# Performance work log

Measured on AMD Instinct MI355X. Metric: run time of the kernel, lower is better.

## Reference

```python
import jax, jax.numpy as jnp
import numpy as np

DIM = 256
NUM_HEADS = 4
HEAD_DIM = DIM // NUM_HEADS
LN_EPS = 1e-5


def setup_inputs() -> dict:
    key = jax.random.key(0)
    ks = jax.random.split(key, 5)
    B, C, H, W = 4, DIM, 64, 64
    x = jax.random.normal(ks[0], (B, C, H, W), dtype=jnp.float32)
    ln_g = jnp.ones((DIM,), dtype=jnp.float32)
    ln_b = jnp.zeros((DIM,), dtype=jnp.float32)
    # torch Linear init scale ~ 1/sqrt(fan_in)
    w_qkv = jax.random.normal(ks[1], (DIM, 3 * DIM), dtype=jnp.float32) / np.sqrt(DIM)
    w_proj = jax.random.normal(ks[2], (DIM, DIM), dtype=jnp.float32) / np.sqrt(DIM)
    b_proj = jax.random.normal(ks[3], (DIM,), dtype=jnp.float32) * 0.01
    return {"x": x, "ln_g": ln_g, "ln_b": ln_b, "w_qkv": w_qkv,
            "w_proj": w_proj, "b_proj": b_proj}


def _attention_block(x, ln_g, ln_b, w_qkv, w_proj, b_proj):
    B, C, H, W = x.shape
    N = H * W
    h, d = NUM_HEADS, HEAD_DIM
    # b c h w -> b n c
    t = x.reshape(B, C, N).transpose(0, 2, 1)
    # LayerNorm over channel dim
    mu = jnp.mean(t, axis=-1, keepdims=True)
    var = jnp.mean(jnp.square(t - mu), axis=-1, keepdims=True)
    t = (t - mu) * jax.lax.rsqrt(var + LN_EPS) * ln_g + ln_b
    # qkv projection (no bias); layout of last dim is (three, heads, d)
    qkv = t @ w_qkv  # [B, N, 3*C]
    qkv = qkv.reshape(B, N, 3, h, d)
    q = qkv[:, :, 0].transpose(0, 2, 1, 3)  # [B, h, N, d]
    k = qkv[:, :, 1].transpose(0, 2, 1, 3)
    v = qkv[:, :, 2].transpose(0, 2, 1, 3)
    # scaled dot-product attention (original chunks over queries; same math)
    scale = 1.0 / jnp.sqrt(jnp.asarray(d, dtype=q.dtype))
    dots = jnp.einsum('bhnd,bhmd->bhnm', q, k) * scale
    attn = jax.nn.softmax(dots, axis=-1)
    o = jnp.einsum('bhnm,bhmd->bhnd', attn, v)  # [B, h, N, d]
    # b h n d -> b n (h d)
    o = o.transpose(0, 2, 1, 3).reshape(B, N, C)
    o = o @ w_proj.T + b_proj  # torch Linear convention not needed; keep explicit
    # b n c -> b c h w
    return o.transpose(0, 2, 1).reshape(B, C, H, W)


def reference(x, ln_g, ln_b, w_qkv, w_proj, b_proj):
    return _attention_block(x, ln_g, ln_b, w_qkv, w_proj, b_proj)
```

## Files before the change

kernel.cpp:

```cpp
#include <hip/hip_runtime.h>
#include <math.h>

#define NB 4
#define NC 256
#define NHEADS 4
#define DH 64
#define NT 4096
#define QSCALE (0.125f * 1.44269504088896f)

typedef __bf16  bf16x8 __attribute__((ext_vector_type(8)));
typedef float   f32x4  __attribute__((ext_vector_type(4)));
typedef float   f32x16 __attribute__((ext_vector_type(16)));
typedef short   s16x8  __attribute__((ext_vector_type(8)));
typedef unsigned int u32x4 __attribute__((ext_vector_type(4)));

static __device__ __forceinline__ unsigned short f2bf(float f) {
    unsigned u = __float_as_uint(f);
    u = (u + 0x7fffu + ((u >> 16) & 1u)) >> 16;
    return (unsigned short)u;
}

static __device__ __forceinline__ float fast_exp2(float x) {
    return __builtin_amdgcn_exp2f(x);
}

static __device__ __forceinline__ unsigned cvtpk(float lo, float hi) {
    unsigned r;
    asm("v_cvt_pk_bf16_f32 %0, %1, %2" : "=v"(r) : "v"(lo), "v"(hi));
    return r;
}

static __device__ __forceinline__ void plswap(unsigned &a, unsigned &b) {
    asm("v_permlane32_swap_b32 %0, %1" : "+v"(a), "+v"(b));
}

static __device__ __forceinline__ bf16x8 as_bf16x8(u32x4 v) {
    return __builtin_bit_cast(bf16x8, v);
}

static __device__ __forceinline__ void gload16(const unsigned short* g, unsigned short* l) {
    __builtin_amdgcn_global_load_lds((const __attribute__((address_space(1))) void*)g,
                                     (__attribute__((address_space(3))) void*)l, 16, 0, 0);
}

static __device__ __forceinline__ void stage_64x256(
    unsigned short* __restrict__ lds, const unsigned short* __restrict__ g, int tid)
{
    #pragma unroll
    for (int chunk = 0; chunk < 8; ++chunk) {
        const int row = chunk * 8 + (tid >> 5);
        const int col = (tid & 31) * 8;
        *(s16x8*)&lds[row * 264 + col] = *(const s16x8*)&g[row * 256 + col];
    }
}

__global__ __launch_bounds__(256) void k_prep(
    const float* __restrict__ wqkv, const float* __restrict__ wproj,
    unsigned short* __restrict__ wqkv_t, unsigned short* __restrict__ wproj_bf)
{
    const int id = blockIdx.x;
    const int tid = threadIdx.x;
    if (id < 48) {
        __shared__ float T[64][65];
        const int jt = id % 12, ct = id / 12;
        #pragma unroll
        for (int p = 0; p < 16; ++p) {
            const int idx = tid + (p << 8);
            const int r = idx >> 6, cl = idx & 63;
            T[r][cl] = wqkv[(size_t)(ct * 64 + r) * 768 + jt * 64 + cl];
        }
        __syncthreads();
        #pragma unroll
        for (int p = 0; p < 16; ++p) {
            const int idx = tid + (p << 8);
            const int r = idx >> 6, cl = idx & 63;
            wqkv_t[(size_t)(jt * 64 + r) * 256 + ct * 64 + cl] = f2bf(T[cl][r]);
        }
    } else {
        const int base = (id - 48) * 2048 + tid * 8;
        s16x8 v;
        #pragma unroll
        for (int j = 0; j < 8; ++j) v[j] = (short)f2bf(wproj[base + j]);
        *(s16x8*)&wproj_bf[base] = v;
    }
}

__global__ __launch_bounds__(256) void k_ln_qkv(
    const float* __restrict__ x,
    const float* __restrict__ ln_g,
    const float* __restrict__ ln_b,
    const unsigned short* __restrict__ wqkv_t,
    unsigned short* __restrict__ q_bf,
    unsigned short* __restrict__ k_bf,
    unsigned short* __restrict__ v_bf)
{
    __shared__ unsigned short An[64 * 264];
    __shared__ unsigned short Wt[64 * 264];
    __shared__ float red1[4][64], red2[4][64];
    __shared__ float mu_s[64], rs_s[64];

    const int b     = blockIdx.x >> 6;
    const int n0    = (blockIdx.x & 63) << 6;
    const int tid   = threadIdx.x;
    const int li    = tid & 63;
    const int grp   = tid >> 6;
    const int w     = grp;
    const int lane  = li;
    const int q4    = lane >> 4;
    const int c     = lane & 15;

    const float* xb = x + ((size_t)b * NC) * NT + n0 + li;

    float xr[64];
    #pragma unroll
    for (int chunk = 0; chunk < 8; ++chunk)
        #pragma unroll
        for (int j = 0; j < 8; ++j)
            xr[chunk * 8 + j] = xb[(size_t)(chunk * 32 + grp * 8 + j) * NT];

    float s1 = 0.f, s2 = 0.f;
    #pragma unroll
    for (int i = 0; i < 64; ++i) { s1 += xr[i]; s2 += xr[i] * xr[i]; }
    red1[grp][li] = s1; red2[grp][li] = s2;
    __syncthreads();
    if (tid < 64) {
        const float t1 = red1[0][tid] + red1[1][tid] + red1[2][tid] + red1[3][tid];
        const float t2 = red2[0][tid] + red2[1][tid] + red2[2][tid] + red2[3][tid];
        const float mu  = t1 * (1.0f / NC);
        const float var = t2 * (1.0f / NC) - mu * mu;
        mu_s[tid] = mu;
        rs_s[tid] = rsqrtf(var + 1e-5f);
    }
    __syncthreads();
    const float mu = mu_s[li];
    const float rs = rs_s[li];

    #pragma unroll
    for (int chunk = 0; chunk < 8; ++chunk) {
        s16x8 pk;
        #pragma unroll
        for (int j = 0; j < 8; ++j) {
            const int ch = chunk * 32 + grp * 8 + j;
            const float vv = (xr[chunk * 8 + j] - mu) * rs * ln_g[ch] + ln_b[ch];
            pk[j] = (short)f2bf(vv);
        }
        *(s16x8*)&An[li * 264 + chunk * 32 + grp * 8] = pk;
    }
    __syncthreads();

    bf16x8 aT[8];
    #pragma unroll
    for (int kt = 0; kt < 8; ++kt)
        aT[kt] = *(const bf16x8*)&An[(16 * w + c) * 264 + kt * 32 + q4 * 8];

    for (int three = 0; three < 3; ++three) {
        for (int jt = 0; jt < 4; ++jt) {
            __syncthreads();
            stage_64x256(Wt, wqkv_t + (size_t)(three * 256 + jt * 64) * 256, tid);
            __syncthreads();

            f32x4 acc[4];
            #pragma unroll
            for (int nt = 0; nt < 4; ++nt)
                #pragma unroll
                for (int r = 0; r < 4; ++r) acc[nt][r] = 0.f;

            const int bh = b * NHEADS + jt;
            if (three < 2) {
                #pragma unroll
                for (int nt = 0; nt < 4; ++nt)
                    #pragma unroll
                    for (int kt = 0; kt < 8; ++kt) {
                        const bf16x8 bb = *(const bf16x8*)&Wt[(16 * nt + c) * 264 + kt * 32 + q4 * 8];
                        acc[nt] = __builtin_amdgcn_mfma_f32_16x16x32_bf16(aT[kt], bb, acc[nt], 0, 0, 0);
                    }
                unsigned short* dst = (three == 0 ? q_bf : k_bf) + ((size_t)bh * NT + n0) * DH;
                const float sc = (three == 0) ? QSCALE : 1.0f;
                #pragma unroll
                for (int nt = 0; nt < 4; ++nt)
                    #pragma unroll
                    for (int r = 0; r < 4; ++r)
                        dst[(size_t)(16 * w + 4 * q4 + r) * DH + 16 * nt + c] = f2bf(acc[nt][r] * sc);
            } else {
                bf16x8 aW[8];
                #pragma unroll
                for (int kt = 0; kt < 8; ++kt)
                    aW[kt] = *(const bf16x8*)&Wt[(16 * w + c) * 264 + kt * 32 + q4 * 8];
                #pragma unroll
                for (int nt = 0; nt < 4; ++nt)
                    #pragma unroll
                    for (int kt = 0; kt < 8; ++kt) {
                        const bf16x8 bb = *(const bf16x8*)&An[(16 * nt + c) * 264 + kt * 32 + q4 * 8];
                        acc[nt] = __builtin_amdgcn_mfma_f32_16x16x32_bf16(aW[kt], bb, acc[nt], 0, 0, 0);
                    }
                unsigned short* dst = v_bf + (size_t)bh * DH * NT;
                #pragma unroll
                for (int nt = 0; nt < 4; ++nt)
                    #pragma unroll
                    for (int r = 0; r < 4; ++r)
                        dst[(size_t)(16 * w + 4 * q4 + r) * NT + n0 + 16 * nt + c] = f2bf(acc[nt][r]);
            }
        }
    }
}

__global__ __launch_bounds__(256, 2) void k_attn(
    const unsigned short* __restrict__ qg,
    const unsigned short* __restrict__ kg,
    const unsigned short* __restrict__ vg,
    unsigned short* __restrict__ og)
{
    __shared__ unsigned short Ks[2 * 8192];
    __shared__ unsigned short Vt[2 * 8192];
    __shared__ float l_s[4][32];

    const int bx   = ((blockIdx.x & 7) << 6) | (blockIdx.x >> 3);
    const int bh   = bx >> 5;
    const int qt   = bx & 31;
    const int n0   = qt << 7;
    const int tid  = threadIdx.x;
    const int w    = tid >> 6;
    const int lane = tid & 63;
    const int c5   = lane & 31;
    const int hi   = lane >> 5;
    const int qb   = n0 + (w << 5);
    const int swz  = c5 & 7;

    const unsigned short* kb = kg + (size_t)bh * NT * DH;
    const unsigned short* vb = vg + (size_t)bh * DH * NT;

    bf16x8 aq[4];
    {
        const unsigned short* qrow = qg + ((size_t)bh * NT + qb + c5) * DH + hi * 8;
        #pragma unroll
        for (int ks = 0; ks < 4; ++ks)
            aq[ks] = *(const bf16x8*)(qrow + ks * 16);
    }

    const int rr  = lane >> 3;
    const int kcK = (lane & 7) ^ rr;
    const int rd  = lane >> 4;
    const int ckV = lane & 15;

    #define ISSUE_TILE(it_, bi_)                                               \
        {                                                                      \
            const unsigned short* ktp = kb + (size_t)(it_) * 128 * DH;         \
            const unsigned short* vtp = vb + (size_t)(it_) * 128;              \
            _Pragma("unroll")                                                  \
            for (int t = 0; t < 4; ++t) {                                      \
                const int grp_ = w * 4 + t;                                    \
                gload16(ktp + (size_t)(grp_ * 8 + rr) * DH + kcK * 8,          \
                        &Ks[(bi_) * 8192 + grp_ * 512 + lane * 8]);            \
                const int kcV_ = ckV ^ ((4 * grp_ + rd) & 7);                  \
                gload16(vtp + (size_t)(4 * grp_ + rd) * NT + kcV_ * 8,         \
                        &Vt[(bi_) * 8192 + grp_ * 512 + lane * 8]);            \
            }                                                                  \
        }

    #define QK_SB(sv, sb)                                                      \
        {                                                                      \
            _Pragma("unroll")                                                  \
            for (int ks = 0; ks < 4; ++ks) {                                   \
                const bf16x8 kf = *(const bf16x8*)                             \
                    &Kb[((sb) * 32 + c5) * 64 + (((2 * ks + hi) ^ swz) << 3)]; \
                sv = __builtin_amdgcn_mfma_f32_32x32x16_bf16(kf, aq[ks], sv, 0, 0, 0); \
            }                                                                  \
        }

    #define EXP_SB(sv)                                                         \
        {                                                                      \
            _Pragma("unroll")                                                  \
            for (int r = 0; r < 16; r += 4) {                                  \
                sv[r]   = fast_exp2(sv[r]);   ls0 += sv[r];                    \
                sv[r+1] = fast_exp2(sv[r+1]); ls1 += sv[r+1];                  \
                sv[r+2] = fast_exp2(sv[r+2]); ls2 += sv[r+2];                  \
                sv[r+3] = fast_exp2(sv[r+3]); ls3 += sv[r+3];                  \
            }                                                                  \
        }

    #define PACK_SB(sv, pa0, pa1)                                              \
        {                                                                      \
            unsigned x0 = cvtpk(sv[0], sv[1]),  x1 = cvtpk(sv[4], sv[5]);      \
            plswap(x0, x1);                                                    \
            unsigned x2 = cvtpk(sv[2], sv[3]),  x3 = cvtpk(sv[6], sv[7]);      \
            plswap(x2, x3);                                                    \
            pa0 = (u32x4){x0, x2, x1, x3};                                     \
            unsigned y0 = cvtpk(sv[8], sv[9]),  y1 = cvtpk(sv[12], sv[13]);    \
            plswap(y0, y1);                                                    \
            unsigned y2 = cvtpk(sv[10], sv[11]), y3 = cvtpk(sv[14], sv[15]);   \
            plswap(y2, y3);                                                    \
            pa1 = (u32x4){y0, y2, y1, y3};                                     \
        }

    #define PV_SB(pa0, pa1, sb)                                                \
        {                                                                      \
            _Pragma("unroll")                                                  \
            for (int dt = 0; dt < 2; ++dt) {                                   \
                const int rv = (dt * 32 + c5) * 128;                           \
                const bf16x8 vA = *(const bf16x8*)                             \
                    &Vb[rv + (((4 * (sb) + hi) ^ swz) << 3)];                  \
                oac[dt] = __builtin_amdgcn_mfma_f32_32x32x16_bf16(             \
                    as_bf16x8(pa0), vA, oac[dt], 0, 0, 0);                     \
                const bf16x8 vB = *(const bf16x8*)                             \
                    &Vb[rv + (((4 * (sb) + 2 + hi) ^ swz) << 3)];              \
                oac[dt] = __builtin_amdgcn_mfma_f32_32x32x16_bf16(             \
                    as_bf16x8(pa1), vB, oac[dt], 0, 0, 0);                     \
            }                                                                  \
        }

    ISSUE_TILE(0, 0)

    f32x16 oac[2];
    #pragma unroll
    for (int dt = 0; dt < 2; ++dt)
        #pragma unroll
        for (int r = 0; r < 16; ++r) oac[dt][r] = 0.f;
    float ls0 = 0.f, ls1 = 0.f, ls2 = 0.f, ls3 = 0.f;

    for (int it = 0; it < 32; ++it) {
        const int cur = it & 1;
        asm volatile("s_waitcnt vmcnt(0)\n\ts_barrier" ::: "memory");
        if (it < 31) ISSUE_TILE(it + 1, cur ^ 1)

        const unsigned short* Kb = &Ks[cur * 8192];
        const unsigned short* Vb = &Vt[cur * 8192];

        f32x16 sA, sB, sC, sD;
        #pragma unroll
        for (int r = 0; r < 16; ++r) { sA[r] = 0.f; sB[r] = 0.f; sC[r] = 0.f; sD[r] = 0.f; }

        __builtin_amdgcn_s_setprio(1);
        QK_SB(sA, 0)
        QK_SB(sB, 1)
        QK_SB(sC, 2)
        QK_SB(sD, 3)
        __builtin_amdgcn_s_setprio(0);

        u32x4 a0, a1, b0, b1, c0, c1, d0, d1;
        EXP_SB(sA)
        PACK_SB(sA, a0, a1)
        EXP_SB(sB)
        PV_SB(a0, a1, 0)
        PACK_SB(sB, b0, b1)
        EXP_SB(sC)
        PV_SB(b0, b1, 1)
        PACK_SB(sC, c0, c1)
        EXP_SB(sD)
        PV_SB(c0, c1, 2)
        PACK_SB(sD, d0, d1)
        PV_SB(d0, d1, 3)
    }
    #undef ISSUE_TILE
    #undef QK_SB
    #undef EXP_SB
    #undef PACK_SB
    #undef PV_SB

    const float lsum = (ls0 + ls1) + (ls2 + ls3);
    const float t = lsum + __shfl_xor(lsum, 32);
    if (lane < 32) l_s[w][c5] = t;
    __syncthreads();

    unsigned short* ob = og + ((size_t)bh * NT + qb) * DH;
    #pragma unroll
    for (int r = 0; r < 16; ++r) {
        const int qrow = (r & 3) + 8 * (r >> 2) + 4 * hi;
        const float rn = 1.0f / l_s[w][qrow];
        ob[(size_t)qrow * DH + c5]      = f2bf(oac[0][r] * rn);
        ob[(size_t)qrow * DH + 32 + c5] = f2bf(oac[1][r] * rn);
    }
}

__global__ __launch_bounds__(256) void k_proj(
    const unsigned short* __restrict__ o_bf,
    const unsigned short* __restrict__ wproj_bf,
    const float* __restrict__ b_proj,
    float* __restrict__ out)
{
    __shared__ unsigned short Os[64 * 264];
    __shared__ unsigned short Ws[64 * 264];

    const int b   = blockIdx.x >> 6;
    const int n0  = (blockIdx.x & 63) << 6;
    const int yh  = blockIdx.y;
    const int tid = threadIdx.x;
    const int w   = tid >> 6;
    const int lane = tid & 63;
    const int q4  = lane >> 4;
    const int c   = lane & 15;

    #pragma unroll
    for (int chunk = 0; chunk < 8; ++chunk) {
        const int row = chunk * 8 + (tid >> 5);
        const int col = (tid & 31) * 8;
        const int hd  = col >> 6;
        const int c64 = col & 63;
        const unsigned short* src =
            &o_bf[((size_t)(b * NHEADS + hd) * NT + n0 + row) * DH + c64];
        *(s16x8*)&Os[row * 264 + col] = *(const s16x8*)src;
    }

    for (int ct = 0; ct < 2; ++ct) {
        const int cg0 = (yh * 2 + ct) * 64;
        if (ct) __syncthreads();
        stage_64x256(Ws, wproj_bf + (size_t)cg0 * NC, tid);
        __syncthreads();

        bf16x8 a[8];
        #pragma unroll
        for (int kt = 0; kt < 8; ++kt)
            a[kt] = *(const bf16x8*)&Ws[(16 * w + c) * 264 + kt * 32 + q4 * 8];

        f32x4 acc[4];
        #pragma unroll
        for (int nt = 0; nt < 4; ++nt)
            #pragma unroll
            for (int r = 0; r < 4; ++r) acc[nt][r] = 0.f;

        #pragma unroll
        for (int nt = 0; nt < 4; ++nt)
            #pragma unroll
            for (int kt = 0; kt < 8; ++kt) {
                const bf16x8 bb = *(const bf16x8*)&Os[(16 * nt + c) * 264 + kt * 32 + q4 * 8];
                acc[nt] = __builtin_amdgcn_mfma_f32_16x16x32_bf16(a[kt], bb, acc[nt], 0, 0, 0);
            }

        #pragma unroll
        for (int nt = 0; nt < 4; ++nt)
            #pragma unroll
            for (int r = 0; r < 4; ++r) {
                const int cg = cg0 + 16 * w + 4 * q4 + r;
                out[((size_t)b * NC + cg) * NT + n0 + 16 * nt + c] = acc[nt][r] + b_proj[cg];
            }
    }
}

extern "C" void kernel_launch(void* const* d_in, const int* in_sizes, int n_in,
                              void* d_out, int out_size, void* d_ws, size_t ws_size,
                              hipStream_t stream)
{
    const float* x      = (const float*)d_in[0];
    const float* ln_g   = (const float*)d_in[1];
    const float* ln_b   = (const float*)d_in[2];
    const float* w_qkv  = (const float*)d_in[3];
    const float* w_proj = (const float*)d_in[4];
    const float* b_proj = (const float*)d_in[5];
    float* out = (float*)d_out;

    const size_t TEN = (size_t)NB * NHEADS * NT * DH;

    unsigned short* ws16 = (unsigned short*)d_ws;
    unsigned short* q_bf    = ws16;
    unsigned short* k_bf    = ws16 + TEN;
    unsigned short* v_bf    = ws16 + 2 * TEN;
    unsigned short* o_bf    = ws16 + 3 * TEN;
    unsigned short* wqkv_t  = ws16 + 4 * TEN;
    unsigned short* wproj_b = wqkv_t + 768 * 256;

    k_prep<<<80, 256, 0, stream>>>(w_qkv, w_proj, wqkv_t, wproj_b);
    k_ln_qkv<<<NB * 64, 256, 0, stream>>>(x, ln_g, ln_b, wqkv_t, q_bf, k_bf, v_bf);
    k_attn<<<512, 256, 0, stream>>>(q_bf, k_bf, v_bf, o_bf);
    k_proj<<<dim3(NB * 64, 2), 256, 0, stream>>>(o_bf, wproj_b, b_proj, out);
}
```

Measured before the change: 182.9 us.

## Process 64 query rows per wave in attention to reuse K/V fragments

Each wave now handles two 32-row query groups, so every K and V fragment read from LDS feeds two MFMAs. The attention grid drops from 512 to 256 blocks of 256 query rows, and launch bounds change to one block per SIMD group. The goal is to halve LDS traffic and global K/V loads per unit of work. The cost is many more registers (four score accumulators, four output accumulators), lower occupancy, and only 256 blocks, which may underfill a 256-CU device with little latency hiding.

New measurement: 201.1 us. +10.0%, slower.

```diff
diff --git a/kernel.cpp b/kernel.cpp
--- a/kernel.cpp
+++ b/kernel.cpp
@@ -204,7 +204,7 @@
     }
 }
 
-__global__ __launch_bounds__(256, 2) void k_attn(
+__global__ __launch_bounds__(256, 1) void k_attn(
     const unsigned short* __restrict__ qg,
     const unsigned short* __restrict__ kg,
     const unsigned short* __restrict__ vg,
@@ -212,29 +212,31 @@
 {
     __shared__ unsigned short Ks[2 * 8192];
     __shared__ unsigned short Vt[2 * 8192];
-    __shared__ float l_s[4][32];
-
-    const int bx   = ((blockIdx.x & 7) << 6) | (blockIdx.x >> 3);
-    const int bh   = bx >> 5;
-    const int qt   = bx & 31;
-    const int n0   = qt << 7;
+    __shared__ float l_s[4][64];
+
+    const int bx   = ((blockIdx.x & 7) << 5) | (blockIdx.x >> 3);
+    const int bh   = bx >> 4;
+    const int qt   = bx & 15;
+    const int n0   = qt << 8;
     const int tid  = threadIdx.x;
     const int w    = tid >> 6;
     const int lane = tid & 63;
     const int c5   = lane & 31;
     const int hi   = lane >> 5;
-    const int qb   = n0 + (w << 5);
+    const int qb   = n0 + (w << 6);
     const int swz  = c5 & 7;
 
     const unsigned short* kb = kg + (size_t)bh * NT * DH;
     const unsigned short* vb = vg + (size_t)bh * DH * NT;
 
-    bf16x8 aq[4];
-    {
-        const unsigned short* qrow = qg + ((size_t)bh * NT + qb + c5) * DH + hi * 8;
+    bf16x8 aq[2][4];
+    #pragma unroll
+    for (int g = 0; g < 2; ++g) {
+        const unsigned short* qrow =
+            qg + ((size_t)bh * NT + qb + 32 * g + c5) * DH + hi * 8;
         #pragma unroll
         for (int ks = 0; ks < 4; ++ks)
-            aq[ks] = *(const bf16x8*)(qrow + ks * 16);
+            aq[g][ks] = *(const bf16x8*)(qrow + ks * 16);
     }
 
     const int rr  = lane >> 3;
@@ -257,24 +259,25 @@
             }                                                                  \
         }
 
-    #define QK_SB(sv, sb)                                                      \
+    #define QK_SB2(sv0, sv1, sb)                                               \
         {                                                                      \
             _Pragma("unroll")                                                  \
             for (int ks = 0; ks < 4; ++ks) {                                   \
                 const bf16x8 kf = *(const bf16x8*)                             \
                     &Kb[((sb) * 32 + c5) * 64 + (((2 * ks + hi) ^ swz) << 3)]; \
-                sv = __builtin_amdgcn_mfma_f32_32x32x16_bf16(kf, aq[ks], sv, 0, 0, 0); \
+                sv0 = __builtin_amdgcn_mfma_f32_32x32x16_bf16(kf, aq[0][ks], sv0, 0, 0, 0); \
+                sv1 = __builtin_amdgcn_mfma_f32_32x32x16_bf16(kf, aq[1][ks], sv1, 0, 0, 0); \
             }                                                                  \
         }
 
-    #define EXP_SB(sv)                                                         \
+    #define EXP_SB(sv, g)                                                      \
         {                                                                      \
             _Pragma("unroll")                                                  \
             for (int r = 0; r < 16; r += 4) {                                  \
-                sv[r]   = fast_exp2(sv[r]);   ls0 += sv[r];                    \
-                sv[r+1] = fast_exp2(sv[r+1]); ls1 += sv[r+1];                  \
-                sv[r+2] = fast_exp2(sv[r+2]); ls2 += sv[r+2];                  \
-                sv[r+3] = fast_exp2(sv[r+3]); ls3 += sv[r+3];                  \
+                sv[r]   = fast_exp2(sv[r]);   lsg[g][0] += sv[r];              \
+                sv[r+1] = fast_exp2(sv[r+1]); lsg[g][1] += sv[r+1];            \
+                sv[r+2] = fast_exp2(sv[r+2]); lsg[g][2] += sv[r+2];            \
+                sv[r+3] = fast_exp2(sv[r+3]); lsg[g][3] += sv[r+3];            \
             }                                                                  \
         }
 
@@ -292,30 +295,36 @@
             pa1 = (u32x4){y0, y2, y1, y3};                                     \
         }
 
-    #define PV_SB(pa0, pa1, sb)                                                \
+    #define PV_SB2(p00, p01, p10, p11, sb)                                     \
         {                                                                      \
             _Pragma("unroll")                                                  \
             for (int dt = 0; dt < 2; ++dt) {                                   \
                 const int rv = (dt * 32 + c5) * 128;                           \
                 const bf16x8 vA = *(const bf16x8*)                             \
                     &Vb[rv + (((4 * (sb) + hi) ^ swz) << 3)];                  \
-                oac[dt] = __builtin_amdgcn_mfma_f32_32x32x16_bf16(             \
-                    as_bf16x8(pa0), vA, oac[dt], 0, 0, 0);                     \
+                oac[0][dt] = __builtin_amdgcn_mfma_f32_32x32x16_bf16(          \
+                    as_bf16x8(p00), vA, oac[0][dt], 0, 0, 0);                  \
+                oac[1][dt] = __builtin_amdgcn_mfma_f32_32x32x16_bf16(          \
+                    as_bf16x8(p10), vA, oac[1][dt], 0, 0, 0);                  \
                 const bf16x8 vB = *(const bf16x8*)                             \
                     &Vb[rv + (((4 * (sb) + 2 + hi) ^ swz) << 3)];              \
-                oac[dt] = __builtin_amdgcn_mfma_f32_32x32x16_bf16(             \
-                    as_bf16x8(pa1), vB, oac[dt], 0, 0, 0);                     \
+                oac[0][dt] = __builtin_amdgcn_mfma_f32_32x32x16_bf16(          \
+                    as_bf16x8(p01), vB, oac[0][dt], 0, 0, 0);                  \
+                oac[1][dt] = __builtin_amdgcn_mfma_f32_32x32x16_bf16(          \
+                    as_bf16x8(p11), vB, oac[1][dt], 0, 0, 0);                  \
             }                                                                  \
         }
 
     ISSUE_TILE(0, 0)
 
-    f32x16 oac[2];
-    #pragma unroll
-    for (int dt = 0; dt < 2; ++dt)
-        #pragma unroll
-        for (int r = 0; r < 16; ++r) oac[dt][r] = 0.f;
-    float ls0 = 0.f, ls1 = 0.f, ls2 = 0.f, ls3 = 0.f;
+    f32x16 oac[2][2];
+    #pragma unroll
+    for (int g = 0; g < 2; ++g)
+        #pragma unroll
+        for (int dt = 0; dt < 2; ++dt)
+            #pragma unroll
+            for (int r = 0; r < 16; ++r) oac[g][dt][r] = 0.f;
+    float lsg[2][4] = {};
 
     for (int it = 0; it < 32; ++it) {
         const int cur = it & 1;
@@ -325,50 +334,60 @@
         const unsigned short* Kb = &Ks[cur * 8192];
         const unsigned short* Vb = &Vt[cur * 8192];
 
-        f32x16 sA, sB, sC, sD;
-        #pragma unroll
-        for (int r = 0; r < 16; ++r) { sA[r] = 0.f; sB[r] = 0.f; sC[r] = 0.f; sD[r] = 0.f; }
-
-        __builtin_amdgcn_s_setprio(1);
-        QK_SB(sA, 0)
-        QK_SB(sB, 1)
-        QK_SB(sC, 2)
-        QK_SB(sD, 3)
-        __builtin_amdgcn_s_setprio(0);
-
-        u32x4 a0, a1, b0, b1, c0, c1, d0, d1;
-        EXP_SB(sA)
-        PACK_SB(sA, a0, a1)
-        EXP_SB(sB)
-        PV_SB(a0, a1, 0)
-        PACK_SB(sB, b0, b1)
-        EXP_SB(sC)
-        PV_SB(b0, b1, 1)
-        PACK_SB(sC, c0, c1)
-        EXP_SB(sD)
-        PV_SB(c0, c1, 2)
-        PACK_SB(sD, d0, d1)
-        PV_SB(d0, d1, 3)
+        #pragma unroll
+        for (int hf = 0; hf < 2; ++hf) {
+            const int sb0 = 2 * hf, sb1 = 2 * hf + 1;
+
+            f32x16 s00, s01, s10, s11;
+            #pragma unroll
+            for (int r = 0; r < 16; ++r) { s00[r]=0.f; s01[r]=0.f; s10[r]=0.f; s11[r]=0.f; }
+
+            __builtin_amdgcn_s_setprio(1);
+            QK_SB2(s00, s01, sb0)
+            QK_SB2(s10, s11, sb1)
+            __builtin_amdgcn_s_setprio(0);
+
+            EXP_SB(s00, 0)
+            EXP_SB(s01, 1)
+            EXP_SB(s10, 0)
+            EXP_SB(s11, 1)
+
+            u32x4 p00a, p00b, p01a, p01b, p10a, p10b, p11a, p11b;
+            PACK_SB(s00, p00a, p00b)
+            PACK_SB(s01, p01a, p01b)
+            PACK_SB(s10, p10a, p10b)
+            PACK_SB(s11, p11a, p11b)
+
+            __builtin_amdgcn_s_setprio(1);
+            PV_SB2(p00a, p00b, p01a, p01b, sb0)
+            PV_SB2(p10a, p10b, p11a, p11b, sb1)
+            __builtin_amdgcn_s_setprio(0);
+        }
     }
     #undef ISSUE_TILE
-    #undef QK_SB
+    #undef QK_SB2
     #undef EXP_SB
     #undef PACK_SB
-    #undef PV_SB
-
-    const float lsum = (ls0 + ls1) + (ls2 + ls3);
-    const float t = lsum + __shfl_xor(lsum, 32);
-    if (lane < 32) l_s[w][c5] = t;
+    #undef PV_SB2
+
+    #pragma unroll
+    for (int g = 0; g < 2; ++g) {
+        const float lsum = (lsg[g][0] + lsg[g][1]) + (lsg[g][2] + lsg[g][3]);
+        const float t = lsum + __shfl_xor(lsum, 32);
+        if (lane < 32) l_s[w][32 * g + c5] = t;
+    }
     __syncthreads();
 
     unsigned short* ob = og + ((size_t)bh * NT + qb) * DH;
     #pragma unroll
-    for (int r = 0; r < 16; ++r) {
-        const int qrow = (r & 3) + 8 * (r >> 2) + 4 * hi;
-        const float rn = 1.0f / l_s[w][qrow];
-        ob[(size_t)qrow * DH + c5]      = f2bf(oac[0][r] * rn);
-        ob[(size_t)qrow * DH + 32 + c5] = f2bf(oac[1][r] * rn);
-    }
+    for (int g = 0; g < 2; ++g)
+        #pragma unroll
+        for (int r = 0; r < 16; ++r) {
+            const int qrow = (r & 3) + 8 * (r >> 2) + 4 * hi;
+            const float rn = 1.0f / l_s[w][32 * g + qrow];
+            ob[(size_t)(32 * g + qrow) * DH + c5]      = f2bf(oac[g][0][r] * rn);
+            ob[(size_t)(32 * g + qrow) * DH + 32 + c5] = f2bf(oac[g][1][r] * rn);
+        }
 }
 
 __global__ __launch_bounds__(256) void k_proj(
@@ -459,6 +478,6 @@
 
     k_prep<<<80, 256, 0, stream>>>(w_qkv, w_proj, wqkv_t, wproj_b);
     k_ln_qkv<<<NB * 64, 256, 0, stream>>>(x, ln_g, ln_b, wqkv_t, q_bf, k_bf, v_bf);
-    k_attn<<<512, 256, 0, stream>>>(q_bf, k_bf, v_bf, o_bf);
+    k_attn<<<256, 256, 0, stream>>>(q_bf, k_bf, v_bf, o_bf);
     k_proj<<<dim3(NB * 64, 2), 256, 0, stream>>>(o_bf, wproj_b, b_proj, out);
 }
```
